# Performance work log

Measured on AMD Instinct MI355X. Metric: run time of the kernel, lower is better.

The kernel has to match this reference:

```python
import jax, jax.numpy as jnp
import numpy as np

B, T, TKV, D, H = 4, 2048, 512, 1024, 16
HD = D // H  # 64
HIDDEN = ((int(D * 4 * 2 / 3) + 7) // 8) * 8  # 2736
EPS = 1e-6


def setup_inputs() -> dict:
    key = jax.random.key(0)
    ks = jax.random.split(key, 16)
    x = jax.random.normal(ks[0], (B, T, D), jnp.float32)
    memory = jax.random.normal(ks[1], (B, TKV, D), jnp.float32)
    # RoPE frequencies: (T, HD//2, 2) = (cos, sin)
    inv_freq = 1.0 / (10000.0 ** (jnp.arange(0, HD, 2, dtype=jnp.float32) / HD))
    angles = jnp.arange(T, dtype=jnp.float32)[:, None] * inv_freq[None, :]
    freqs_cis = jnp.stack([jnp.cos(angles), jnp.sin(angles)], axis=-1)
    # causal mask (T, T): 0 on/below diag, -inf above
    causal_mask = jnp.where(jnp.tril(jnp.ones((T, T), bool)), 0.0, -jnp.inf).astype(jnp.float32)
    s = 0.02
    w = lambda k, i, o: jax.random.normal(k, (i, o), jnp.float32) * s  # stored as (in, out)
    return {
        'x': x, 'memory': memory, 'freqs_cis': freqs_cis, 'causal_mask': causal_mask,
        'sa_wq': w(ks[2], D, D), 'sa_wk': w(ks[3], D, D), 'sa_wv': w(ks[4], D, D), 'sa_wo': w(ks[5], D, D),
        'ca_wq': w(ks[6], D, D), 'ca_wk': w(ks[7], D, D), 'ca_wv': w(ks[8], D, D), 'ca_wo': w(ks[9], D, D),
        'w1': w(ks[10], D, HIDDEN), 'w3': w(ks[11], D, HIDDEN), 'w2': w(ks[12], HIDDEN, D),
        'g_sa': jnp.ones((D,), jnp.float32), 'g_ca': jnp.ones((D,), jnp.float32), 'g_ffn': jnp.ones((D,), jnp.float32),
    }


def rmsnorm(x, g):
    return x * jax.lax.rsqrt(jnp.mean(x * x, axis=-1, keepdims=True) + EPS) * g


def apply_rope(t, f):
    # t: (B, H, T, HD); f: (T, HD//2, 2)
    tr = t.reshape(*t.shape[:-1], HD // 2, 2)
    a, b = tr[..., 0], tr[..., 1]
    cos, sin = f[None, None, :, :, 0], f[None, None, :, :, 1]
    out = jnp.stack([a * cos - b * sin, a * sin + b * cos], axis=-1)
    return out.reshape(t.shape)


def heads(x, w):
    # (B, S, D) @ (D, D) -> (B, H, S, HD)
    b, s, _ = x.shape
    return (x @ w).reshape(b, s, H, HD).transpose(0, 2, 1, 3)


def attention(xq, kv, wq, wk, wv, wo, freqs=None, mask=None):
    q, k, v = heads(xq, wq), heads(kv, wk), heads(kv, wv)
    if freqs is not None:
        q, k = apply_rope(q, freqs), apply_rope(k, freqs)
    attn = jnp.einsum('bhqd,bhkd->bhqk', q, k) * (HD ** -0.5)
    if mask is not None:
        attn = attn + mask
    attn = jax.nn.softmax(attn, axis=-1)
    out = jnp.einsum('bhqk,bhkd->bhqd', attn, v)
    out = out.transpose(0, 2, 1, 3).reshape(xq.shape[0], xq.shape[1], D)
    return out @ wo


def reference(x, memory, freqs_cis, causal_mask,
              sa_wq, sa_wk, sa_wv, sa_wo,
              ca_wq, ca_wk, ca_wv, ca_wo,
              w1, w2, w3, g_sa, g_ca, g_ffn):
    x = rmsnorm(x + attention(x, x, sa_wq, sa_wk, sa_wv, sa_wo, freqs=freqs_cis, mask=causal_mask), g_sa)
    x = rmsnorm(x + attention(x, memory, ca_wq, ca_wk, ca_wv, ca_wo), g_ca)
    ffn = (jax.nn.silu(x @ w1) * (x @ w3)) @ w2
    x = rmsnorm(x + ffn, g_ffn)
    return x
```

## Files before the change

### kernel.cpp

```cpp
#include <hip/hip_runtime.h>
#include <hip/hip_bf16.h>

typedef __attribute__((ext_vector_type(8))) short s16x8;
typedef __attribute__((ext_vector_type(4))) float f32x4;
typedef __attribute__((ext_vector_type(16))) float f32x16;
typedef unsigned short u16;
typedef unsigned int u32;
typedef unsigned long long u64;

#define MFMA(a,b,c) __builtin_amdgcn_mfma_f32_16x16x32_bf16(a,b,c,0,0,0)
#define MFMA32(a,b,c) __builtin_amdgcn_mfma_f32_32x32x16_bf16(a,b,c,0,0,0)

constexpr int B_ = 4, T_ = 2048, TKV_ = 512, D_ = 1024, H_ = 16, HD_ = 64;
constexpr int HID_ = 2736, HIDP_ = 2816;

__device__ __forceinline__ float bf2f(u16 x) {
    union { float f; u32 u; } c; c.u = ((u32)x) << 16; return c.f;
}
__device__ __forceinline__ u16 f2bf(float f) {
    union { float f; u32 u; } c; c.f = f;
    u32 r = c.u + 0x7fffu + ((c.u >> 16) & 1u);
    return (u16)(r >> 16);
}

__device__ __forceinline__ void gload16(const void* g, void* l) {
    __builtin_amdgcn_global_load_lds(
        (const __attribute__((address_space(1))) u32*)g,
        (__attribute__((address_space(3))) u32*)l, 16, 0, 0);
}

__global__ __launch_bounds__(256) void wt_cast(const float* __restrict__ W, u16* __restrict__ WT,
                                               int K, int N, int Kp, int Np) {
    __shared__ float t[32][33];
    int tid = threadIdx.x;
    int tx = tid & 31, ty = tid >> 5;
    int n0 = blockIdx.x * 32, k0 = blockIdx.y * 32;
#pragma unroll
    for (int i = 0; i < 4; ++i) {
        int kk = k0 + ty + i * 8, nn = n0 + tx;
        t[ty + i * 8][tx] = (kk < K && nn < N) ? W[(size_t)kk * N + nn] : 0.f;
    }
    __syncthreads();
#pragma unroll
    for (int i = 0; i < 4; ++i) {
        int nn = n0 + ty + i * 8, kk = k0 + tx;
        WT[(size_t)nn * Kp + kk] = f2bf(t[tx][ty + i * 8]);
    }
}

__global__ __launch_bounds__(256) void cast_bf16(const float* __restrict__ in, u16* __restrict__ out, int n4) {
    int i = blockIdx.x * 256 + threadIdx.x;
    if (i >= n4) return;
    float4 v = ((const float4*)in)[i];
    u64 pk = (u64)f2bf(v.x) | ((u64)f2bf(v.y) << 16) | ((u64)f2bf(v.z) << 32) | ((u64)f2bf(v.w) << 48);
    ((u64*)out)[i] = pk;
}

__device__ __forceinline__ void gemm_store(void* C, const u16* mul, size_t idx, float v, int mode) {
    if (mode == 0) {
        ((float*)C)[idx] = v;
    } else if (mode == 1) {
        ((u16*)C)[idx] = f2bf(v);
    } else if (mode == 2) {
        float sg = 1.f / (1.f + __expf(-v));
        ((u16*)C)[idx] = f2bf(v * sg);
    } else if (mode == 3) {
        float h = bf2f(mul[idx]);
        ((u16*)C)[idx] = f2bf(v * h);
    } else {
        ((u16*)C)[idx] = f2bf(v * 0.125f);
    }
}


__global__ __launch_bounds__(256) void gemm_bf16(const u16* __restrict__ A, const u16* __restrict__ Bt,
                                                 void* __restrict__ C, const u16* __restrict__ mul,
                                                 int M, int N, int K, int mode, int nwg) {
    __shared__ __align__(16) u16 As[128 * 64];
    __shared__ __align__(16) u16 Bs[128 * 64];
    const int tid = threadIdx.x;
    const int lane = tid & 63, wid = tid >> 6;
    const int wr = wid >> 1, wc = wid & 1;
    const int li = lane & 15, g = lane >> 4;

    int bid = (int)blockIdx.x;
    bid = (bid & 7) * (nwg >> 3) + (bid >> 3);

    const int tn = N >> 7;
    const int m0 = (bid / tn) * 128, n0 = (bid % tn) * 128;

    const int rowst = tid >> 3;
    const int colb = (((tid & 7) ^ ((tid >> 3) & 7)) * 16);
    const char* ga = (const char*)A + ((size_t)(m0 + rowst) * K) * 2 + colb;
    const char* gb = (const char*)Bt + ((size_t)(n0 + rowst) * K) * 2 + colb;
    const size_t rstride = (size_t)32 * K * 2;

    f32x4 acc[4][4] = {};
    const int nt = K >> 6;

    for (int t = 0; t < nt; ++t) {
#pragma unroll
        for (int i = 0; i < 4; ++i) {
            gload16(ga + (size_t)t * 128 + i * rstride, (char*)As + i * 4096 + wid * 1024);
            gload16(gb + (size_t)t * 128 + i * rstride, (char*)Bs + i * 4096 + wid * 1024);
        }
        __syncthreads();
#pragma unroll
        for (int kk = 0; kk < 2; ++kk) {
            s16x8 aF[4], bF[4];
            const int sl = ((kk << 2) | g) ^ (li & 7);
#pragma unroll
            for (int m = 0; m < 4; ++m) aF[m] = *(const s16x8*)&As[(wr * 64 + m * 16 + li) * 64 + sl * 8];
#pragma unroll
            for (int n = 0; n < 4; ++n) bF[n] = *(const s16x8*)&Bs[(wc * 64 + n * 16 + li) * 64 + sl * 8];
#pragma unroll
            for (int m = 0; m < 4; ++m)
#pragma unroll
                for (int n = 0; n < 4; ++n)
                    acc[m][n] = MFMA(aF[m], bF[n], acc[m][n]);
        }
        __syncthreads();
    }

#pragma unroll
    for (int m = 0; m < 4; ++m)
#pragma unroll
        for (int n = 0; n < 4; ++n)
#pragma unroll
            for (int r = 0; r < 4; ++r) {
                size_t row = m0 + wr * 64 + m * 16 + g * 4 + r;
                size_t col = n0 + wc * 64 + n * 16 + li;
                gemm_store(C, mul, row * N + col, acc[m][n][r], mode);
            }
}

__global__ __launch_bounds__(256) void gemm_w13(const u16* __restrict__ A, const u16* __restrict__ B1t,
                                                const u16* __restrict__ B3t, u16* __restrict__ Hout,
                                                int M, int N, int K, int nwg) {
    __shared__ __align__(16) u16 As[128 * 64];
    __shared__ __align__(16) u16 B1s[128 * 64];
    __shared__ __align__(16) u16 B3s[128 * 64];
    const int tid = threadIdx.x;
    const int lane = tid & 63, wid = tid >> 6;
    const int wr = wid >> 1, wc = wid & 1;
    const int li = lane & 15, g = lane >> 4;

    int bid = (int)blockIdx.x;
    bid = (bid & 7) * (nwg >> 3) + (bid >> 3);

    const int tn = N >> 7;
    const int m0 = (bid / tn) * 128, n0 = (bid % tn) * 128;

    const int rowst = tid >> 3;
    const int colb = (((tid & 7) ^ ((tid >> 3) & 7)) * 16);
    const char* ga = (const char*)A + ((size_t)(m0 + rowst) * K) * 2 + colb;
    const char* gb1 = (const char*)B1t + ((size_t)(n0 + rowst) * K) * 2 + colb;
    const char* gb3 = (const char*)B3t + ((size_t)(n0 + rowst) * K) * 2 + colb;
    const size_t rstride = (size_t)32 * K * 2;

    f32x4 acc1[4][4] = {}, acc3[4][4] = {};
    const int nt = K >> 6;

    for (int t = 0; t < nt; ++t) {
#pragma unroll
        for (int i = 0; i < 4; ++i) {
            gload16(ga + (size_t)t * 128 + i * rstride, (char*)As + i * 4096 + wid * 1024);
            gload16(gb1 + (size_t)t * 128 + i * rstride, (char*)B1s + i * 4096 + wid * 1024);
            gload16(gb3 + (size_t)t * 128 + i * rstride, (char*)B3s + i * 4096 + wid * 1024);
        }
        __syncthreads();
#pragma unroll
        for (int kk = 0; kk < 2; ++kk) {
            const int sl = ((kk << 2) | g) ^ (li & 7);
            s16x8 aF[4];
#pragma unroll
            for (int m = 0; m < 4; ++m) aF[m] = *(const s16x8*)&As[(wr * 64 + m * 16 + li) * 64 + sl * 8];
            {
                s16x8 bF[4];
#pragma unroll
                for (int n = 0; n < 4; ++n) bF[n] = *(const s16x8*)&B1s[(wc * 64 + n * 16 + li) * 64 + sl * 8];
#pragma unroll
                for (int m = 0; m < 4; ++m)
#pragma unroll
                    for (int n = 0; n < 4; ++n)
                        acc1[m][n] = MFMA(aF[m], bF[n], acc1[m][n]);
            }
            {
                s16x8 bF[4];
#pragma unroll
                for (int n = 0; n < 4; ++n) bF[n] = *(const s16x8*)&B3s[(wc * 64 + n * 16 + li) * 64 + sl * 8];
#pragma unroll
                for (int m = 0; m < 4; ++m)
#pragma unroll
                    for (int n = 0; n < 4; ++n)
                        acc3[m][n] = MFMA(aF[m], bF[n], acc3[m][n]);
            }
        }
        __syncthreads();
    }

#pragma unroll
    for (int m = 0; m < 4; ++m)
#pragma unroll
        for (int n = 0; n < 4; ++n)
#pragma unroll
            for (int r = 0; r < 4; ++r) {
                size_t row = m0 + wr * 64 + m * 16 + g * 4 + r;
                size_t col = n0 + wc * 64 + n * 16 + li;
                float h1 = acc1[m][n][r];
                float h3 = acc3[m][n][r];
                float sg = 1.f / (1.f + __expf(-h1));
                Hout[row * N + col] = f2bf(h1 * sg * h3);
            }
}

__global__ __launch_bounds__(256) void rope_qk(u16* __restrict__ q, u16* __restrict__ k,
                                               const float* __restrict__ fr, int S) {
    size_t idx = (size_t)blockIdx.x * 256 + threadIdx.x;
    int i = (int)(idx & 31);
    int h = (int)((idx >> 5) & 15);
    size_t bt = idx >> 9;
    int t = (int)(bt & (T_ - 1));
    float2 cs = ((const float2*)fr)[t * 32 + i];
    size_t off = bt * (size_t)S + h * 64 + 2 * i;
    {
        u32* p = (u32*)(q + off);
        u32 w = *p;
        float a = bf2f((u16)(w & 0xffff)), b = bf2f((u16)(w >> 16));
        *p = (u32)f2bf((a * cs.x - b * cs.y) * 0.125f) | ((u32)f2bf((a * cs.y + b * cs.x) * 0.125f) << 16);
    }
    {
        u32* p = (u32*)(k + off);
        u32 w = *p;
        float a = bf2f((u16)(w & 0xffff)), b = bf2f((u16)(w >> 16));
        *p = (u32)f2bf(a * cs.x - b * cs.y) | ((u32)f2bf(a * cs.y + b * cs.x) << 16);
    }
}

__global__ __launch_bounds__(256) void vtrans(const u16* __restrict__ v, u16* __restrict__ vT,
                                              int Tk, int S) {
    __shared__ u16 tile[32][34];
    int bh = blockIdx.x;
    int t0 = blockIdx.y * 32, d0 = blockIdx.z * 32;
    int b = bh >> 4, h = bh & 15;
    int tid = threadIdx.x;
    int tx = tid & 31, ty = tid >> 5;
#pragma unroll
    for (int i = 0; i < 4; ++i)
        tile[ty + i * 8][tx] = v[((size_t)b * Tk + t0 + ty + i * 8) * S + h * 64 + d0 + tx];
    __syncthreads();
#pragma unroll
    for (int i = 0; i < 4; ++i)
        vT[((size_t)bh * 64 + d0 + ty + i * 8) * Tk + t0 + tx] = tile[tx][ty + i * 8];
}

__device__ __forceinline__ void sm_pack(const f32x16& s, int hi, float& mr, float& lr,
                                        f32x16& o0, f32x16& o1, s16x8& pf0v, s16x8& pf1v) {
    float bm = fmaxf(fmaxf(fmaxf(s[0], s[1]), fmaxf(s[2], s[3])),
                     fmaxf(fmaxf(s[4], s[5]), fmaxf(s[6], s[7])));
    float bm2 = fmaxf(fmaxf(fmaxf(s[8], s[9]), fmaxf(s[10], s[11])),
                      fmaxf(fmaxf(s[12], s[13]), fmaxf(s[14], s[15])));
    bm = fmaxf(bm, bm2);
    bm = fmaxf(bm, __shfl_xor(bm, 32));
    float mn = fmaxf(mr, bm);
    float sc = __expf(mr - mn);
    mr = mn;
    float p[16];
    float rs = 0.f;
#pragma unroll
    for (int r = 0; r < 16; ++r) { p[r] = __expf(s[r] - mn); rs += p[r]; }
    rs += __shfl_xor(rs, 32);
    lr = lr * sc + rs;
#pragma unroll
    for (int r = 0; r < 16; ++r) { o0[r] *= sc; o1[r] *= sc; }

    u32 pk[8];
#pragma unroll
    for (int i = 0; i < 8; ++i)
        pk[i] = (u32)f2bf(p[2 * i]) | ((u32)f2bf(p[2 * i + 1]) << 16);
    u32 e1 = __shfl_xor(hi ? pk[0] : pk[2], 32);
    u32 e2 = __shfl_xor(hi ? pk[1] : pk[3], 32);
    u32 e3 = __shfl_xor(hi ? pk[4] : pk[6], 32);
    u32 e4 = __shfl_xor(hi ? pk[5] : pk[7], 32);
    union { s16x8 v; u32 w[4]; } pf0, pf1;
    pf0.w[0] = hi ? e1 : pk[0];
    pf0.w[1] = hi ? e2 : pk[1];
    pf0.w[2] = hi ? pk[2] : e1;
    pf0.w[3] = hi ? pk[3] : e2;
    pf1.w[0] = hi ? e3 : pk[4];
    pf1.w[1] = hi ? e4 : pk[5];
    pf1.w[2] = hi ? pk[6] : e3;
    pf1.w[3] = hi ? pk[7] : e4;
    pf0v = pf0.v;
    pf1v = pf1.v;
}

__device__ __forceinline__ void attn_out(u16* ob, const f32x16& o0, const f32x16& o1,
                                         float lr, int hi) {
    float inv = 1.f / lr;
#pragma unroll
    for (int r = 0; r < 16; ++r) {
        int hd = (r & 3) + 8 * (r >> 2) + 4 * hi;
        ob[hd] = f2bf(o0[r] * inv);
        ob[hd + 32] = f2bf(o1[r] * inv);
    }
}

__device__ __forceinline__ void attn32(const u16* __restrict__ qh, const u16* __restrict__ kh,
                                       const u16* __restrict__ vh, u16* __restrict__ oh,
                                       int q0, int nkb, int Tk, int causal, int lq, int hi,
                                       int QS, int KS) {
    const u16* qb = qh + (size_t)(q0 + lq) * QS;
    s16x8 qf[4];
#pragma unroll
    for (int c = 0; c < 4; ++c) qf[c] = *(const s16x8*)&qb[c * 16 + hi * 8];

    f32x16 o0 = {}, o1 = {};
    float mr = -1e30f, lr = 0.f;

    for (int kb = 0; kb < nkb; ++kb) {
        const int ks = kb * 32;
        f32x16 s = {};
        const u16* kp = kh + (size_t)(ks + lq) * KS + hi * 8;
#pragma unroll
        for (int c = 0; c < 4; ++c) {
            s16x8 kf = *(const s16x8*)&kp[c * 16];
            s = MFMA32(kf, qf[c], s);
        }
        if (causal && kb == nkb - 1) {
#pragma unroll
            for (int r = 0; r < 16; ++r) {
                int kl = (r & 3) + 8 * (r >> 2) + 4 * hi;
                if (kl > lq) s[r] = -1e30f;
            }
        }
        s16x8 pf0, pf1;
        sm_pack(s, hi, mr, lr, o0, o1, pf0, pf1);

        const u16* v0 = vh + (size_t)lq * Tk + ks + hi * 8;
        const u16* v1 = vh + (size_t)(32 + lq) * Tk + ks + hi * 8;
        o0 = MFMA32(*(const s16x8*)&v0[0],  pf0, o0);
        o0 = MFMA32(*(const s16x8*)&v0[16], pf1, o0);
        o1 = MFMA32(*(const s16x8*)&v1[0],  pf0, o1);
        o1 = MFMA32(*(const s16x8*)&v1[16], pf1, o1);
    }
    attn_out(oh + (size_t)(q0 + lq) * D_, o0, o1, lr, hi);
}

__global__ __launch_bounds__(256) void attn_causal_pair(const u16* __restrict__ q, const u16* __restrict__ k,
                                                        const u16* __restrict__ vT, u16* __restrict__ o,
                                                        int Tq, int Tk, int QS, int KS) {
    const int lane = threadIdx.x & 63, wid = threadIdx.x >> 6;
    const int lq = lane & 31, hi = lane >> 5;
    const int ntile = Tq / 32;
    const int ppb = (ntile / 2) / 4;
    const int bh = blockIdx.x / ppb;
    const int p = (blockIdx.x % ppb) * 4 + wid;
    const int b = bh >> 4, h = bh & 15;

    const u16* qh = q + ((size_t)b * Tq) * QS + h * 64;
    const u16* kh = k + ((size_t)b * Tk) * KS + h * 64;
    const u16* vh = vT + ((size_t)bh * 64) * Tk;
    u16* oh = o + ((size_t)b * Tq) * D_ + h * 64;

    const int tA = p, tB = ntile - 1 - p;
    const int q0A = tA * 32, q0B = tB * 32;

    s16x8 qfA[4], qfB[4];
    {
        const u16* qbA = qh + (size_t)(q0A + lq) * QS;
        const u16* qbB = qh + (size_t)(q0B + lq) * QS;
#pragma unroll
        for (int c = 0; c < 4; ++c) {
            qfA[c] = *(const s16x8*)&qbA[c * 16 + hi * 8];
            qfB[c] = *(const s16x8*)&qbB[c * 16 + hi * 8];
        }
    }

    f32x16 oA0 = {}, oA1 = {}, oB0 = {}, oB1 = {};
    float mrA = -1e30f, lrA = 0.f, mrB = -1e30f, lrB = 0.f;

    for (int kb = 0; kb <= tB; ++kb) {
        const int ks = kb * 32;
        const bool doA = (kb <= tA);
        const u16* kp = kh + (size_t)(ks + lq) * KS + hi * 8;
        s16x8 kf[4];
#pragma unroll
        for (int c = 0; c < 4; ++c) kf[c] = *(const s16x8*)&kp[c * 16];

        f32x16 sA = {}, sB = {};
        if (doA) {
#pragma unroll
            for (int c = 0; c < 4; ++c) sA = MFMA32(kf[c], qfA[c], sA);
        }
#pragma unroll
        for (int c = 0; c < 4; ++c) sB = MFMA32(kf[c], qfB[c], sB);

        const u16* v0p = vh + (size_t)lq * Tk + ks + hi * 8;
        const u16* v1p = vh + (size_t)(32 + lq) * Tk + ks + hi * 8;
        s16x8 v00 = *(const s16x8*)&v0p[0],  v01 = *(const s16x8*)&v0p[16];
        s16x8 v10 = *(const s16x8*)&v1p[0],  v11 = *(const s16x8*)&v1p[16];

        if (doA) {
            if (kb == tA) {
#pragma unroll
                for (int r = 0; r < 16; ++r) {
                    int kl = (r & 3) + 8 * (r >> 2) + 4 * hi;
                    if (kl > lq) sA[r] = -1e30f;
                }
            }
            s16x8 pf0, pf1;
            sm_pack(sA, hi, mrA, lrA, oA0, oA1, pf0, pf1);
            oA0 = MFMA32(v00, pf0, oA0);
            oA0 = MFMA32(v01, pf1, oA0);
            oA1 = MFMA32(v10, pf0, oA1);
            oA1 = MFMA32(v11, pf1, oA1);
        }
        {
            if (kb == tB) {
#pragma unroll
                for (int r = 0; r < 16; ++r) {
                    int kl = (r & 3) + 8 * (r >> 2) + 4 * hi;
                    if (kl > lq) sB[r] = -1e30f;
                }
            }
            s16x8 pf0, pf1;
            sm_pack(sB, hi, mrB, lrB, oB0, oB1, pf0, pf1);
            oB0 = MFMA32(v00, pf0, oB0);
            oB0 = MFMA32(v01, pf1, oB0);
            oB1 = MFMA32(v10, pf0, oB1);
            oB1 = MFMA32(v11, pf1, oB1);
        }
    }

    attn_out(oh + (size_t)(q0A + lq) * D_, oA0, oA1, lrA, hi);
    attn_out(oh + (size_t)(q0B + lq) * D_, oB0, oB1, lrB, hi);
}

__global__ __launch_bounds__(256) void attn_plain32(const u16* __restrict__ q, const u16* __restrict__ k,
                                                    const u16* __restrict__ vT, u16* __restrict__ o,
                                                    int Tq, int Tk, int QS, int KS) {
    const int lane = threadIdx.x & 63, wid = threadIdx.x >> 6;
    const int lq = lane & 31, hi = lane >> 5;
    const int tpb = (Tq / 32) / 4;
    const int bh = blockIdx.x / tpb;
    const int qt = (blockIdx.x % tpb) * 4 + wid;
    const int b = bh >> 4, h = bh & 15;

    const u16* qh = q + ((size_t)b * Tq) * QS + h * 64;
    const u16* kh = k + ((size_t)b * Tk) * KS + h * 64;
    const u16* vh = vT + ((size_t)bh * 64) * Tk;
    u16* oh = o + ((size_t)b * Tq) * D_ + h * 64;

    attn32(qh, kh, vh, oh, qt * 32, Tk / 32, Tk, 0, lq, hi, QS, KS);
}

__global__ __launch_bounds__(256) void addnorm(const float* __restrict__ xa, const u16* __restrict__ xb,
                                               const float* __restrict__ gg, float* __restrict__ fo,
                                               u16* __restrict__ bo) {
    int row = blockIdx.x * 4 + (threadIdx.x >> 6);
    int lane = threadIdx.x & 63;
    const float4* pa = (const float4*)(xa + (size_t)row * D_);
    const u64* pb = (const u64*)(xb + (size_t)row * D_);
    float4 v[4];
    float ss = 0.f;
#pragma unroll
    for (int j = 0; j < 4; ++j) {
        float4 a = pa[lane + 64 * j];
        u64 bw = pb[lane + 64 * j];
        v[j].x = a.x + bf2f((u16)(bw));
        v[j].y = a.y + bf2f((u16)(bw >> 16));
        v[j].z = a.z + bf2f((u16)(bw >> 32));
        v[j].w = a.w + bf2f((u16)(bw >> 48));
        ss += v[j].x * v[j].x + v[j].y * v[j].y + v[j].z * v[j].z + v[j].w * v[j].w;
    }
    ss += __shfl_xor(ss, 1);
    ss += __shfl_xor(ss, 2);
    ss += __shfl_xor(ss, 4);
    ss += __shfl_xor(ss, 8);
    ss += __shfl_xor(ss, 16);
    ss += __shfl_xor(ss, 32);
    float s = rsqrtf(ss * (1.0f / D_) + 1e-6f);
#pragma unroll
    for (int j = 0; j < 4; ++j) {
        float4 gv = ((const float4*)gg)[lane + 64 * j];
        float yx = v[j].x * s * gv.x, yy = v[j].y * s * gv.y;
        float yz = v[j].z * s * gv.z, yw = v[j].w * s * gv.w;
        if (fo) {
            float4 o4; o4.x = yx; o4.y = yy; o4.z = yz; o4.w = yw;
            ((float4*)(fo + (size_t)row * D_))[lane + 64 * j] = o4;
        }
        if (bo) {
            u64 pk = (u64)f2bf(yx) | ((u64)f2bf(yy) << 16) | ((u64)f2bf(yz) << 32) | ((u64)f2bf(yw) << 48);
            ((u64*)(bo + (size_t)row * D_))[lane + 64 * j] = pk;
        }
    }
}

extern "C" void kernel_launch(void* const* d_in, const int* in_sizes, int n_in,
                              void* d_out, int out_size, void* d_ws, size_t ws_size,
                              hipStream_t stream) {
    const float* x    = (const float*)d_in[0];
    const float* mem  = (const float*)d_in[1];
    const float* fr   = (const float*)d_in[2];
    const float* wsaq = (const float*)d_in[4];
    const float* wsak = (const float*)d_in[5];
    const float* wsav = (const float*)d_in[6];
    const float* wsao = (const float*)d_in[7];
    const float* wcaq = (const float*)d_in[8];
    const float* wcak = (const float*)d_in[9];
    const float* wcav = (const float*)d_in[10];
    const float* wcao = (const float*)d_in[11];
    const float* w1   = (const float*)d_in[12];
    const float* w3   = (const float*)d_in[13];
    const float* w2   = (const float*)d_in[14];
    const float* g_sa = (const float*)d_in[15];
    const float* g_ca = (const float*)d_in[16];
    const float* g_ff = (const float*)d_in[17];
    float* outF = (float*)d_out;

    char* p = (char*)d_ws;
    auto alloc = [&](size_t bytes) { char* r = p; p += (bytes + 255) & ~(size_t)255; return r; };
    const size_t DD2 = (size_t)1024 * 1024 * 2;
    u16* wqkvT = (u16*)alloc(3 * DD2);
    u16* saoT  = (u16*)alloc(DD2);
    u16* caqT  = (u16*)alloc(DD2);
    u16* wkvT  = (u16*)alloc(2 * DD2);
    u16* caoT  = (u16*)alloc(DD2);
    u16* w1T   = (u16*)alloc((size_t)HIDP_ * 1024 * 2);
    u16* w3T   = (u16*)alloc((size_t)HIDP_ * 1024 * 2);
    u16* w2T   = (u16*)alloc((size_t)1024 * HIDP_ * 2);
    u16* Ab    = (u16*)alloc((size_t)8192 * 1024 * 2);
    u16* memb  = (u16*)alloc((size_t)2048 * 1024 * 2);
    char* qkvRaw = alloc((size_t)8192 * 3072 * 2);
    u16* qkvb = (u16*)qkvRaw;
    u16* kvb  = (u16*)qkvRaw;
    u16* caqb = (u16*)(qkvRaw + (size_t)25165824);
    u16* vtb  = (u16*)alloc((size_t)8192 * 1024 * 2);
    u16* ob   = (u16*)alloc((size_t)8192 * 1024 * 2);
    u16* Pb   = (u16*)alloc((size_t)8192 * 1024 * 2);
    float* Rf = (float*)alloc((size_t)8192 * 1024 * 4);
    u16* Hb   = (u16*)alloc((size_t)8192 * HIDP_ * 2);

    dim3 blk(256);

    wt_cast<<<dim3(32, 32), blk, 0, stream>>>(wsaq, wqkvT,               1024, 1024, 1024, 1024);
    wt_cast<<<dim3(32, 32), blk, 0, stream>>>(wsak, wqkvT + 1024 * 1024, 1024, 1024, 1024, 1024);
    wt_cast<<<dim3(32, 32), blk, 0, stream>>>(wsav, wqkvT + 2048 * 1024, 1024, 1024, 1024, 1024);
    wt_cast<<<dim3(32, 32), blk, 0, stream>>>(wsao, saoT, 1024, 1024, 1024, 1024);
    wt_cast<<<dim3(32, 32), blk, 0, stream>>>(wcaq, caqT, 1024, 1024, 1024, 1024);
    wt_cast<<<dim3(32, 32), blk, 0, stream>>>(wcak, wkvT,               1024, 1024, 1024, 1024);
    wt_cast<<<dim3(32, 32), blk, 0, stream>>>(wcav, wkvT + 1024 * 1024, 1024, 1024, 1024, 1024);
    wt_cast<<<dim3(32, 32), blk, 0, stream>>>(wcao, caoT, 1024, 1024, 1024, 1024);
    wt_cast<<<dim3(88, 32), blk, 0, stream>>>(w1, w1T, 1024, HID_, 1024, HIDP_);
    wt_cast<<<dim3(88, 32), blk, 0, stream>>>(w3, w3T, 1024, HID_, 1024, HIDP_);
    wt_cast<<<dim3(32, 88), blk, 0, stream>>>(w2, w2T, HID_, 1024, HIDP_, 1024);

    cast_bf16<<<8192, blk, 0, stream>>>(x, Ab, 2097152);
    cast_bf16<<<2048, blk, 0, stream>>>(mem, memb, 524288);

    gemm_bf16<<<1536, blk, 0, stream>>>(Ab, wqkvT, qkvb, nullptr, 8192, 3072, 1024, 1, 1536);
    rope_qk<<<16384, blk, 0, stream>>>(qkvb, qkvb + 1024, fr, 3072);
    vtrans<<<dim3(64, 64, 2), blk, 0, stream>>>(qkvb + 2048, vtb, 2048, 3072);
    attn_causal_pair<<<512, blk, 0, stream>>>(qkvb, qkvb + 1024, vtb, ob, 2048, 2048, 3072, 3072);
    gemm_bf16<<<512, blk, 0, stream>>>(ob, saoT, Pb, nullptr, 8192, 1024, 1024, 1, 512);
    addnorm<<<2048, blk, 0, stream>>>(x, Pb, g_sa, Rf, Ab);

    gemm_bf16<<<512, blk, 0, stream>>>(Ab, caqT, caqb, nullptr, 8192, 1024, 1024, 4, 512);
    gemm_bf16<<<256, blk, 0, stream>>>(memb, wkvT, kvb, nullptr, 2048, 2048, 1024, 1, 256);
    vtrans<<<dim3(64, 16, 2), blk, 0, stream>>>(kvb + 1024, vtb, 512, 2048);
    attn_plain32<<<1024, blk, 0, stream>>>(caqb, kvb, vtb, ob, 2048, 512, 1024, 2048);
    gemm_bf16<<<512, blk, 0, stream>>>(ob, caoT, Pb, nullptr, 8192, 1024, 1024, 1, 512);
    addnorm<<<2048, blk, 0, stream>>>(Rf, Pb, g_ca, Rf, Ab);

    gemm_w13<<<1408, blk, 0, stream>>>(Ab, w1T, w3T, Hb, 8192, HIDP_, 1024, 1408);
    gemm_bf16<<<512, blk, 0, stream>>>(Hb, w2T, Pb, nullptr, 8192, 1024, HIDP_, 1, 512);
    addnorm<<<2048, blk, 0, stream>>>(Rf, Pb, g_ff, outF, nullptr);
}
```

Before: 776.9 us.

## Fuse RoPE into QKV GEMM epilogue and pair query tiles in cross-attention

The QKV projection GEMM gains a mode that applies rotary embedding and the query scaling in its epilogue, using a lane shuffle to fetch the paired element. This removes the separate rope_qk kernel and its read-modify-write pass over Q and K. Cross-attention now processes two query tiles per wave, so each K and V fragment load is reused for both tiles, and half as many blocks are launched. The paired kernel holds more accumulators, which raises register pressure, and the epilogue does extra per-element index math and frequency-table loads.

```diff
diff --git a/kernel.cpp b/kernel.cpp
--- a/kernel.cpp
+++ b/kernel.cpp
@@ -75,6 +75,7 @@
 
 __global__ __launch_bounds__(256) void gemm_bf16(const u16* __restrict__ A, const u16* __restrict__ Bt,
                                                  void* __restrict__ C, const u16* __restrict__ mul,
+                                                 const float* __restrict__ fr,
                                                  int M, int N, int K, int mode, int nwg) {
     __shared__ __align__(16) u16 As[128 * 64];
     __shared__ __align__(16) u16 Bs[128 * 64];
@@ -122,16 +123,45 @@
         __syncthreads();
     }
 
-#pragma unroll
-    for (int m = 0; m < 4; ++m)
-#pragma unroll
-        for (int n = 0; n < 4; ++n)
-#pragma unroll
-            for (int r = 0; r < 4; ++r) {
-                size_t row = m0 + wr * 64 + m * 16 + g * 4 + r;
-                size_t col = n0 + wc * 64 + n * 16 + li;
-                gemm_store(C, mul, row * N + col, acc[m][n][r], mode);
-            }
+    if (mode == 5) {
+#pragma unroll
+        for (int m = 0; m < 4; ++m)
+#pragma unroll
+            for (int n = 0; n < 4; ++n)
+#pragma unroll
+                for (int r = 0; r < 4; ++r) {
+                    size_t row = m0 + wr * 64 + m * 16 + g * 4 + r;
+                    size_t col = n0 + wc * 64 + n * 16 + li;
+                    float v = acc[m][n][r];
+                    int region = (int)(col >> 10);
+                    float out;
+                    if (region < 2) {
+                        float pv = __shfl_xor(v, 1);
+                        int t = (int)(row & (T_ - 1));
+                        int i = ((int)col & 63) >> 1;
+                        float2 cs = ((const float2*)fr)[t * 32 + i];
+                        bool even = ((col & 1) == 0);
+                        float a = even ? v : pv;
+                        float b = even ? pv : v;
+                        out = even ? (a * cs.x - b * cs.y) : (a * cs.y + b * cs.x);
+                        if (region == 0) out *= 0.125f;
+                    } else {
+                        out = v;
+                    }
+                    ((u16*)C)[row * N + col] = f2bf(out);
+                }
+    } else {
+#pragma unroll
+        for (int m = 0; m < 4; ++m)
+#pragma unroll
+            for (int n = 0; n < 4; ++n)
+#pragma unroll
+                for (int r = 0; r < 4; ++r) {
+                    size_t row = m0 + wr * 64 + m * 16 + g * 4 + r;
+                    size_t col = n0 + wc * 64 + n * 16 + li;
+                    gemm_store(C, mul, row * N + col, acc[m][n][r], mode);
+                }
+    }
 }
 
 __global__ __launch_bounds__(256) void gemm_w13(const u16* __restrict__ A, const u16* __restrict__ B1t,
@@ -212,29 +242,6 @@
                 float sg = 1.f / (1.f + __expf(-h1));
                 Hout[row * N + col] = f2bf(h1 * sg * h3);
             }
-}
-
-__global__ __launch_bounds__(256) void rope_qk(u16* __restrict__ q, u16* __restrict__ k,
-                                               const float* __restrict__ fr, int S) {
-    size_t idx = (size_t)blockIdx.x * 256 + threadIdx.x;
-    int i = (int)(idx & 31);
-    int h = (int)((idx >> 5) & 15);
-    size_t bt = idx >> 9;
-    int t = (int)(bt & (T_ - 1));
-    float2 cs = ((const float2*)fr)[t * 32 + i];
-    size_t off = bt * (size_t)S + h * 64 + 2 * i;
-    {
-        u32* p = (u32*)(q + off);
-        u32 w = *p;
-        float a = bf2f((u16)(w & 0xffff)), b = bf2f((u16)(w >> 16));
-        *p = (u32)f2bf((a * cs.x - b * cs.y) * 0.125f) | ((u32)f2bf((a * cs.y + b * cs.x) * 0.125f) << 16);
-    }
-    {
-        u32* p = (u32*)(k + off);
-        u32 w = *p;
-        float a = bf2f((u16)(w & 0xffff)), b = bf2f((u16)(w >> 16));
-        *p = (u32)f2bf(a * cs.x - b * cs.y) | ((u32)f2bf(a * cs.y + b * cs.x) << 16);
-    }
 }
 
 __global__ __launch_bounds__(256) void vtrans(const u16* __restrict__ v, u16* __restrict__ vT,
@@ -306,47 +313,6 @@
     }
 }
 
-__device__ __forceinline__ void attn32(const u16* __restrict__ qh, const u16* __restrict__ kh,
-                                       const u16* __restrict__ vh, u16* __restrict__ oh,
-                                       int q0, int nkb, int Tk, int causal, int lq, int hi,
-                                       int QS, int KS) {
-    const u16* qb = qh + (size_t)(q0 + lq) * QS;
-    s16x8 qf[4];
-#pragma unroll
-    for (int c = 0; c < 4; ++c) qf[c] = *(const s16x8*)&qb[c * 16 + hi * 8];
-
-    f32x16 o0 = {}, o1 = {};
-    float mr = -1e30f, lr = 0.f;
-
-    for (int kb = 0; kb < nkb; ++kb) {
-        const int ks = kb * 32;
-        f32x16 s = {};
-        const u16* kp = kh + (size_t)(ks + lq) * KS + hi * 8;
-#pragma unroll
-        for (int c = 0; c < 4; ++c) {
-            s16x8 kf = *(const s16x8*)&kp[c * 16];
-            s = MFMA32(kf, qf[c], s);
-        }
-        if (causal && kb == nkb - 1) {
-#pragma unroll
-            for (int r = 0; r < 16; ++r) {
-                int kl = (r & 3) + 8 * (r >> 2) + 4 * hi;
-                if (kl > lq) s[r] = -1e30f;
-            }
-        }
-        s16x8 pf0, pf1;
-        sm_pack(s, hi, mr, lr, o0, o1, pf0, pf1);
-
-        const u16* v0 = vh + (size_t)lq * Tk + ks + hi * 8;
-        const u16* v1 = vh + (size_t)(32 + lq) * Tk + ks + hi * 8;
-        o0 = MFMA32(*(const s16x8*)&v0[0],  pf0, o0);
-        o0 = MFMA32(*(const s16x8*)&v0[16], pf1, o0);
-        o1 = MFMA32(*(const s16x8*)&v1[0],  pf0, o1);
-        o1 = MFMA32(*(const s16x8*)&v1[16], pf1, o1);
-    }
-    attn_out(oh + (size_t)(q0 + lq) * D_, o0, o1, lr, hi);
-}
-
 __global__ __launch_bounds__(256) void attn_causal_pair(const u16* __restrict__ q, const u16* __restrict__ k,
                                                         const u16* __restrict__ vT, u16* __restrict__ o,
                                                         int Tq, int Tk, int QS, int KS) {
@@ -437,14 +403,15 @@
     attn_out(oh + (size_t)(q0B + lq) * D_, oB0, oB1, lrB, hi);
 }
 
-__global__ __launch_bounds__(256) void attn_plain32(const u16* __restrict__ q, const u16* __restrict__ k,
-                                                    const u16* __restrict__ vT, u16* __restrict__ o,
-                                                    int Tq, int Tk, int QS, int KS) {
+__global__ __launch_bounds__(256) void attn_plain_pair(const u16* __restrict__ q, const u16* __restrict__ k,
+                                                       const u16* __restrict__ vT, u16* __restrict__ o,
+                                                       int Tq, int Tk, int QS, int KS) {
     const int lane = threadIdx.x & 63, wid = threadIdx.x >> 6;
     const int lq = lane & 31, hi = lane >> 5;
-    const int tpb = (Tq / 32) / 4;
-    const int bh = blockIdx.x / tpb;
-    const int qt = (blockIdx.x % tpb) * 4 + wid;
+    const int ntile = Tq / 32;
+    const int ppb = (ntile / 2) / 4;
+    const int bh = blockIdx.x / ppb;
+    const int p = (blockIdx.x % ppb) * 4 + wid;
     const int b = bh >> 4, h = bh & 15;
 
     const u16* qh = q + ((size_t)b * Tq) * QS + h * 64;
@@ -452,7 +419,61 @@
     const u16* vh = vT + ((size_t)bh * 64) * Tk;
     u16* oh = o + ((size_t)b * Tq) * D_ + h * 64;
 
-    attn32(qh, kh, vh, oh, qt * 32, Tk / 32, Tk, 0, lq, hi, QS, KS);
+    const int q0A = p * 32, q0B = (p + ntile / 2) * 32;
+
+    s16x8 qfA[4], qfB[4];
+    {
+        const u16* qbA = qh + (size_t)(q0A + lq) * QS;
+        const u16* qbB = qh + (size_t)(q0B + lq) * QS;
+#pragma unroll
+        for (int c = 0; c < 4; ++c) {
+            qfA[c] = *(const s16x8*)&qbA[c * 16 + hi * 8];
+            qfB[c] = *(const s16x8*)&qbB[c * 16 + hi * 8];
+        }
+    }
+
+    f32x16 oA0 = {}, oA1 = {}, oB0 = {}, oB1 = {};
+    float mrA = -1e30f, lrA = 0.f, mrB = -1e30f, lrB = 0.f;
+
+    const int nkb = Tk / 32;
+    for (int kb = 0; kb < nkb; ++kb) {
+        const int ks = kb * 32;
+        const u16* kp = kh + (size_t)(ks + lq) * KS + hi * 8;
+        s16x8 kf[4];
+#pragma unroll
+        for (int c = 0; c < 4; ++c) kf[c] = *(const s16x8*)&kp[c * 16];
+
+        f32x16 sA = {}, sB = {};
+#pragma unroll
+        for (int c = 0; c < 4; ++c) sA = MFMA32(kf[c], qfA[c], sA);
+#pragma unroll
+        for (int c = 0; c < 4; ++c) sB = MFMA32(kf[c], qfB[c], sB);
+
+        const u16* v0p = vh + (size_t)lq * Tk + ks + hi * 8;
+        const u16* v1p = vh + (size_t)(32 + lq) * Tk + ks + hi * 8;
+        s16x8 v00 = *(const s16x8*)&v0p[0],  v01 = *(const s16x8*)&v0p[16];
+        s16x8 v10 = *(const s16x8*)&v1p[0],  v11 = *(const s16x8*)&v1p[16];
+
+        {
+            s16x8 pf0, pf1;
+            sm_pack(sA, hi, mrA, lrA, oA0, oA1, pf0, pf1);
+            oA0 = MFMA32(v00, pf0, oA0);
+            oA0 = MFMA32(v01, pf1, oA0);
+            oA1 = MFMA32(v10, pf0, oA1);
+            oA1 = MFMA32(v11, pf1, oA1);
+        }
+        {
+            s16x8 pf0, pf1;
+            sm_pack(sB, hi, mrB, lrB, oB0, oB1, pf0, pf1);
+            oB0 = MFMA32(v00, pf0, oB0);
+            oB0 = MFMA32(v01, pf1, oB0);
+            oB1 = MFMA32(v10, pf0, oB1);
+            oB1 = MFMA32(v11, pf1, oB1);
+        }
+    }
+
+    attn_out(oh + (size_t)(q0A + lq) * D_, oA0, oA1, lrA, hi);
+    attn_out(oh + (size_t)(q0B + lq) * D_, oB0, oB1, lrB, hi);
 }
 
 __global__ __launch_bounds__(256) void addnorm(const float* __restrict__ xa, const u16* __restrict__ xb,
@@ -559,21 +580,20 @@
     cast_bf16<<<8192, blk, 0, stream>>>(x, Ab, 2097152);
     cast_bf16<<<2048, blk, 0, stream>>>(mem, memb, 524288);
 
-    gemm_bf16<<<1536, blk, 0, stream>>>(Ab, wqkvT, qkvb, nullptr, 8192, 3072, 1024, 1, 1536);
-    rope_qk<<<16384, blk, 0, stream>>>(qkvb, qkvb + 1024, fr, 3072);
+    gemm_bf16<<<1536, blk, 0, stream>>>(Ab, wqkvT, qkvb, nullptr, fr, 8192, 3072, 1024, 5, 1536);
     vtrans<<<dim3(64, 64, 2), blk, 0, stream>>>(qkvb + 2048, vtb, 2048, 3072);
     attn_causal_pair<<<512, blk, 0, stream>>>(qkvb, qkvb + 1024, vtb, ob, 2048, 2048, 3072, 3072);
-    gemm_bf16<<<512, blk, 0, stream>>>(ob, saoT, Pb, nullptr, 8192, 1024, 1024, 1, 512);
+    gemm_bf16<<<512, blk, 0, stream>>>(ob, saoT, Pb, nullptr, nullptr, 8192, 1024, 1024, 1, 512);
     addnorm<<<2048, blk, 0, stream>>>(x, Pb, g_sa, Rf, Ab);
 
-    gemm_bf16<<<512, blk, 0, stream>>>(Ab, caqT, caqb, nullptr, 8192, 1024, 1024, 4, 512);
-    gemm_bf16<<<256, blk, 0, stream>>>(memb, wkvT, kvb, nullptr, 2048, 2048, 1024, 1, 256);
+    gemm_bf16<<<512, blk, 0, stream>>>(Ab, caqT, caqb, nullptr, nullptr, 8192, 1024, 1024, 4, 512);
+    gemm_bf16<<<256, blk, 0, stream>>>(memb, wkvT, kvb, nullptr, nullptr, 2048, 2048, 1024, 1, 256);
     vtrans<<<dim3(64, 16, 2), blk, 0, stream>>>(kvb + 1024, vtb, 512, 2048);
-    attn_plain32<<<1024, blk, 0, stream>>>(caqb, kvb, vtb, ob, 2048, 512, 1024, 2048);
-    gemm_bf16<<<512, blk, 0, stream>>>(ob, caoT, Pb, nullptr, 8192, 1024, 1024, 1, 512);
+    attn_plain_pair<<<512, blk, 0, stream>>>(caqb, kvb, vtb, ob, 2048, 512, 1024, 2048);
+    gemm_bf16<<<512, blk, 0, stream>>>(ob, caoT, Pb, nullptr, nullptr, 8192, 1024, 1024, 1, 512);
     addnorm<<<2048, blk, 0, stream>>>(Rf, Pb, g_ca, Rf, Ab);
 
     gemm_w13<<<1408, blk, 0, stream>>>(Ab, w1T, w3T, Hb, 8192, HIDP_, 1024, 1408);
-    gemm_bf16<<<512, blk, 0, stream>>>(Hb, w2T, Pb, nullptr, 8192, 1024, HIDP_, 1, 512);
+    gemm_bf16<<<512, blk, 0, stream>>>(Hb, w2T, Pb, nullptr, nullptr, 8192, 1024, HIDP_, 1, 512);
     addnorm<<<2048, blk, 0, stream>>>(Rf, Pb, g_ff, outF, nullptr);
 }
```

Result: slower. 832.1 us (+7.1%).
